# Optimization experiments

Measured on AMD Instinct MI355X. Metric: run time of the kernel, lower is better.

Reference implementation:

```python
import jax, jax.numpy as jnp
import numpy as np

N, E, NB, P = 100000, 1600000, 1000, 500000


def gcn_conv(x, edge_index, W, b):
    # PyG GCNConv: add self-loops, symmetric D^-1/2 (A+I) D^-1/2 normalization,
    # linear transform, bias.
    n = x.shape[0]
    loop = jnp.arange(n, dtype=edge_index.dtype)
    src = jnp.concatenate([edge_index[0], loop])
    dst = jnp.concatenate([edge_index[1], loop])
    deg = jax.ops.segment_sum(jnp.ones(src.shape[0], x.dtype), dst, num_segments=n)
    dinv = jnp.where(deg > 0, jax.lax.rsqrt(deg), 0.0)
    norm = dinv[src] * dinv[dst]                       # [E+n]
    xw = x @ W                                          # [n, out]
    out = jax.ops.segment_sum(xw[src] * norm[:, None], dst, num_segments=n)
    return out + b


def setup_inputs() -> dict:
    key = jax.random.key(0)
    ks = jax.random.split(key, 12)
    x = jax.random.normal(ks[0], (N, 27), jnp.float32)
    edge_index = jax.random.randint(ks[1], (2, E), 0, N, dtype=jnp.int32)
    bank = jax.random.normal(ks[2], (NB, 27), jnp.float32)
    node1 = jax.random.randint(ks[3], (P,), 0, N + NB, dtype=jnp.int32)
    node2 = jax.random.randint(ks[4], (P,), 0, N + NB, dtype=jnp.int32)

    def lin(k, fan_in, fan_out):
        s = 1.0 / np.sqrt(fan_in)
        kw, kb = jax.random.split(k)
        W = jax.random.uniform(kw, (fan_in, fan_out), jnp.float32, -s, s)
        b = jax.random.uniform(kb, (fan_out,), jnp.float32, -s, s)
        return W, b

    W1, b1 = lin(ks[5], 27, 60)
    W2, b2 = lin(ks[6], 60, 50)
    Wb, bb = lin(ks[7], 27, 50)
    Wf1, bf1 = lin(ks[8], 100, 40)
    Wf2, bf2 = lin(ks[9], 40, 20)
    Wf3, bf3 = lin(ks[10], 20, 4)
    return dict(x=x, bank=bank, W1=W1, b1=b1, W2=W2, b2=b2, Wb=Wb, bb=bb,
                Wf1=Wf1, bf1=bf1, Wf2=Wf2, bf2=bf2, Wf3=Wf3, bf3=bf3,
                edge_index=edge_index, node1=node1, node2=node2)


def reference(x, bank, W1, b1, W2, b2, Wb, bb, Wf1, bf1, Wf2, bf2, Wf3, bf3,
              edge_index, node1, node2):
    h = gcn_conv(x, edge_index, W1, b1)                 # [N, 60]
    h = gcn_conv(h, edge_index, W2, b2)                 # [N, 50]
    bk = bank @ Wb + bb                                 # [NB, 50]
    allh = jnp.concatenate([h, bk], axis=0)             # [N+NB, 50]
    z = jnp.concatenate([allh[node1], allh[node2]], axis=1)  # [P, 100]
    z = z @ Wf1 + bf1
    z = z @ Wf2 + bf2
    z = z @ Wf3 + bf3                                   # [P, 4]
    return jax.nn.softmax(z, axis=0)                    # softmax over dim 0, as in source
```

## Files before the change

### kernel.cpp

```cpp
#include <hip/hip_runtime.h>
#include <math.h>

#define N_NODES 100000
#define N_EDGES 1600000
#define NB_BANK 1000
#define N_PAIRS 500000

#define BUCK_SHIFT 8
#define BUCK_NODES 256
#define NBUCK 391
#define BCAP 5504
#define EPB 4096
#define NSCAT 391
#define NZB4 489
#define SMASK 0x1FFFF

struct Consts {
  float C[27*8];
  float Rb[27*8];
  float u[8];
  float vg[8];
  float vb[8];
};

__device__ void precompute_body(
    const float* __restrict__ W1, const float* __restrict__ b1,
    const float* __restrict__ W2, const float* __restrict__ b2,
    const float* __restrict__ Wb, const float* __restrict__ bb,
    const float* __restrict__ Wf1, const float* __restrict__ bf1,
    const float* __restrict__ Wf2, const float* __restrict__ bf2,
    const float* __restrict__ Wf3, const float* __restrict__ bf3,
    Consts* __restrict__ cst) {
  __shared__ float A[40*4];
  __shared__ float T[100*4];
  __shared__ float B[60*8];
  __shared__ float cvec[4];
  const int tid = threadIdx.x;
  const int nt = blockDim.x;

  for (int idx = tid; idx < 160; idx += nt) {
    int r = idx >> 2, k = idx & 3;
    float s = 0.f;
    for (int j = 0; j < 20; ++j) s += Wf2[r*20+j] * Wf3[j*4+k];
    A[idx] = s;
  }
  __syncthreads();
  for (int idx = tid; idx < 400; idx += nt) {
    int r = idx >> 2, k = idx & 3;
    float s = 0.f;
    for (int j = 0; j < 40; ++j) s += Wf1[r*40+j] * A[j*4+k];
    T[idx] = s;
  }
  if (tid < 4) {
    float s = bf3[tid];
    for (int j = 0; j < 40; ++j) s += bf1[j] * A[j*4+tid];
    for (int j = 0; j < 20; ++j) s += bf2[j] * Wf3[j*4+tid];
    cvec[tid] = s;
  }
  __syncthreads();
  for (int idx = tid; idx < 480; idx += nt) {
    int r = idx >> 3, k = idx & 7;
    int half = k >> 2, kk = k & 3;
    float s = 0.f;
    for (int j = 0; j < 50; ++j) s += W2[r*50+j] * T[(half*50+j)*4+kk];
    B[idx] = s;
  }
  __syncthreads();
  for (int idx = tid; idx < 456; idx += nt) {
    if (idx < 216) {
      int r = idx >> 3, k = idx & 7;
      float s = 0.f;
      for (int j = 0; j < 60; ++j) s += W1[r*60+j] * B[j*8+k];
      cst->C[idx] = s;
    } else if (idx < 432) {
      int i2 = idx - 216;
      int r = i2 >> 3, k = i2 & 7, half = k >> 2, kk = k & 3;
      float s = 0.f;
      for (int j = 0; j < 50; ++j) s += Wb[r*50+j] * T[(half*50+j)*4+kk];
      cst->Rb[i2] = s;
    } else if (idx < 440) {
      int k = idx - 432;
      float s = 0.f;
      for (int j = 0; j < 60; ++j) s += b1[j] * B[j*8+k];
      cst->u[k] = s;
    } else if (idx < 448) {
      int k = idx - 440, half = k >> 2, kk = k & 3;
      float s = (half == 0) ? cvec[kk] : 0.f;
      for (int j = 0; j < 50; ++j) s += b2[j] * T[(half*50+j)*4+kk];
      cst->vg[k] = s;
    } else {
      int k = idx - 448, half = k >> 2, kk = k & 3;
      float s = (half == 0) ? cvec[kk] : 0.f;
      for (int j = 0; j < 50; ++j) s += bb[j] * T[(half*50+j)*4+kk];
      cst->vb[k] = s;
    }
  }
}

__global__ __launch_bounds__(1024) void k_scatter(
    const int* __restrict__ ei, int* __restrict__ bcnt, int* __restrict__ ebuf,
    const float* __restrict__ W1, const float* __restrict__ b1,
    const float* __restrict__ W2, const float* __restrict__ b2,
    const float* __restrict__ Wb, const float* __restrict__ bb,
    const float* __restrict__ Wf1, const float* __restrict__ bf1,
    const float* __restrict__ Wf2, const float* __restrict__ bf2,
    const float* __restrict__ Wf3, const float* __restrict__ bf3,
    Consts* __restrict__ cst) {
  if (blockIdx.x == NSCAT) {
    precompute_body(W1, b1, W2, b2, Wb, bb, Wf1, bf1, Wf2, bf2, Wf3, bf3, cst);
    return;
  }
  __shared__ int hist[NBUCK];
  __shared__ int base[NBUCK];
  const int t = threadIdx.x;
  const int e0 = blockIdx.x * EPB;
  int dcache[EPB / 1024];
  if (t < NBUCK) hist[t] = 0;
  __syncthreads();
#pragma unroll
  for (int i = 0; i < EPB / 1024; ++i) {
    int e = e0 + i * 1024 + t;
    int d = (e < N_EDGES) ? ei[N_EDGES + e] : -1;
    dcache[i] = d;
    if (d >= 0) atomicAdd(&hist[d >> BUCK_SHIFT], 1);
  }
  __syncthreads();
  if (t < NBUCK) {
    int h = hist[t];
    base[t] = h ? (t * BCAP + atomicAdd(&bcnt[t], h)) : 0;
    hist[t] = 0;
  }
  __syncthreads();
#pragma unroll
  for (int i = 0; i < EPB / 1024; ++i) {
    int e = e0 + i * 1024 + t;
    int d = dcache[i];
    if (d >= 0) {
      int s = ei[e];
      int b = d >> BUCK_SHIFT;
      int pos = base[b] + atomicAdd(&hist[b], 1);
      ebuf[pos] = ((d & (BUCK_NODES - 1)) << 17) | s;
    }
  }
}

__global__ __launch_bounds__(512) void k_degfill_x8(
    const int* __restrict__ bcnt, const int* __restrict__ ebuf,
    const float* __restrict__ x, const Consts* __restrict__ cst,
    float* __restrict__ dinv, int* __restrict__ rbeg, int* __restrict__ rend,
    int* __restrict__ csr, float* __restrict__ Xs) {
  __shared__ int cnt[BUCK_NODES];
  __shared__ int lcur[BUCK_NODES];
  __shared__ float sdinv[BUCK_NODES];
  __shared__ float xs[BUCK_NODES * 27];
  const int b = blockIdx.x;
  const int t = threadIdx.x;
  if (t < BUCK_NODES) cnt[t] = 0;
  __syncthreads();
  const int beg = b * BCAP, end = beg + bcnt[b];
  for (int j = beg + t; j < end; j += 512)
    atomicAdd(&cnt[ebuf[j] >> 17], 1);
  const int xbase = b * (BUCK_NODES * 27);
  for (int j = t; j < BUCK_NODES * 27; j += 512) {
    int g = xbase + j;
    xs[j] = (g < N_NODES * 27) ? x[g] : 0.f;
  }
  __syncthreads();
  int v = (t < BUCK_NODES) ? cnt[t] : 0;
  for (int off = 1; off < BUCK_NODES; off <<= 1) {
    int u = (t < BUCK_NODES && t >= off) ? cnt[t - off] : 0;
    __syncthreads();
    if (t < BUCK_NODES) cnt[t] += u;
    __syncthreads();
  }
  if (t < BUCK_NODES) {
    const int node = (b << BUCK_SHIFT) + t;
    const int excl = beg + cnt[t] - v;
    lcur[t] = excl;
    float dv = rsqrtf((float)v + 1.0f);
    sdinv[t] = dv;
    if (node < N_NODES) {
      rbeg[node] = excl;
      rend[node] = excl + v;
      dinv[node] = dv;
    }
  }
  __syncthreads();
  for (int j = beg + t; j < end; j += 512) {
    int code = ebuf[j];
    int pos = atomicAdd(&lcur[code >> 17], 1);
    csr[pos] = code & SMASK;
  }
  for (int idx = t; idx < BUCK_NODES * 8; idx += 512) {
    int li = idx >> 3, k = idx & 7;
    int node = (b << BUCK_SHIFT) + li;
    if (node < N_NODES) {
      float s = 0.f;
      for (int c = 0; c < 27; ++c) s += xs[li*27+c] * cst->C[c*8+k];
      Xs[(size_t)node*8+k] = s * sdinv[li];
    }
  }
}

__global__ __launch_bounds__(256) void k_gather1(const int* __restrict__ rbeg,
                                                 const int* __restrict__ rend,
                                                 const int* __restrict__ csr,
                                                 const float* __restrict__ dinv,
                                                 const float2* __restrict__ Xs2,
                                                 float2* __restrict__ Ys2,
                                                 float* __restrict__ dvec) {
  int t = blockIdx.x * 256 + threadIdx.x;
  int d = t >> 2, q = t & 3;
  if (d >= N_NODES) return;
  const int beg = rbeg[d], end = rend[d];
  const float nd = dinv[d];
  float2 self = Xs2[d*4 + q];
  float ax = self.x, ay = self.y;
  float dsum = nd;
  int j = beg;
  for (; j + 8 <= end; j += 8) {
    int s0 = csr[j],   s1 = csr[j+1], s2 = csr[j+2], s3 = csr[j+3];
    int s4 = csr[j+4], s5 = csr[j+5], s6 = csr[j+6], s7 = csr[j+7];
    float2 a0 = Xs2[s0*4+q], a1 = Xs2[s1*4+q], a2 = Xs2[s2*4+q], a3 = Xs2[s3*4+q];
    float2 a4 = Xs2[s4*4+q], a5 = Xs2[s5*4+q], a6 = Xs2[s6*4+q], a7 = Xs2[s7*4+q];
    ax += ((a0.x + a1.x) + (a2.x + a3.x)) + ((a4.x + a5.x) + (a6.x + a7.x));
    ay += ((a0.y + a1.y) + (a2.y + a3.y)) + ((a4.y + a5.y) + (a6.y + a7.y));
    if (q == 0)
      dsum += ((dinv[s0] + dinv[s1]) + (dinv[s2] + dinv[s3]))
            + ((dinv[s4] + dinv[s5]) + (dinv[s6] + dinv[s7]));
  }
  for (; j < end; ++j) {
    int s = csr[j];
    float2 a = Xs2[s*4+q];
    ax += a.x; ay += a.y;
    if (q == 0) dsum += dinv[s];
  }
  float nn = nd * nd;
  Ys2[t] = make_float2(nn * ax, nn * ay);
  if (q == 0) dvec[d] = nd * dsum;
}

__global__ __launch_bounds__(256) void k_gather2g(const int* __restrict__ rbeg,
                                                  const int* __restrict__ rend,
                                                  const int* __restrict__ csr,
                                                  const float* __restrict__ dinv,
                                                  const float2* __restrict__ Ys2,
                                                  const float* __restrict__ dvec,
                                                  const float* __restrict__ bank,
                                                  const Consts* __restrict__ cst,
                                                  float2* __restrict__ gall2) {
  int t = blockIdx.x * 256 + threadIdx.x;
  int d = t >> 2, q = t & 3;
  if (d >= N_NODES + NB_BANK) return;
  int c0 = 2*q, c1 = 2*q + 1;
  if (d >= N_NODES) {
    int bk = d - N_NODES;
    float sx = cst->vb[c0], sy = cst->vb[c1];
    for (int cc = 0; cc < 27; ++cc) {
      float bv = bank[bk*27+cc];
      sx += bv * cst->Rb[cc*8+c0];
      sy += bv * cst->Rb[cc*8+c1];
    }
    gall2[t] = make_float2(sx, sy);
    return;
  }
  const int beg = rbeg[d], end = rend[d];
  float2 self = Ys2[d*4 + q];
  float ax = self.x, ay = self.y;
  int j = beg;
  for (; j + 8 <= end; j += 8) {
    int s0 = csr[j],   s1 = csr[j+1], s2 = csr[j+2], s3 = csr[j+3];
    int s4 = csr[j+4], s5 = csr[j+5], s6 = csr[j+6], s7 = csr[j+7];
    float2 a0 = Ys2[s0*4+q], a1 = Ys2[s1*4+q], a2 = Ys2[s2*4+q], a3 = Ys2[s3*4+q];
    float2 a4 = Ys2[s4*4+q], a5 = Ys2[s5*4+q], a6 = Ys2[s6*4+q], a7 = Ys2[s7*4+q];
    ax += ((a0.x + a1.x) + (a2.x + a3.x)) + ((a4.x + a5.x) + (a6.x + a7.x));
    ay += ((a0.y + a1.y) + (a2.y + a3.y)) + ((a4.y + a5.y) + (a6.y + a7.y));
  }
  for (; j < end; ++j) {
    float2 a = Ys2[csr[j]*4+q];
    ax += a.x; ay += a.y;
  }
  float nd = dinv[d], dv = dvec[d];
  gall2[t] = make_float2(nd * ax + dv * cst->u[c0] + cst->vg[c0],
                         nd * ay + dv * cst->u[c1] + cst->vg[c1]);
}

__device__ inline void sm_merge(float4& m1, float4& s1,
                                const float4 m2, const float4 s2) {
  float4 M;
  M.x = fmaxf(m1.x, m2.x); M.y = fmaxf(m1.y, m2.y);
  M.z = fmaxf(m1.z, m2.z); M.w = fmaxf(m1.w, m2.w);
  s1.x = s1.x * expf(m1.x - M.x) + s2.x * expf(m2.x - M.x);
  s1.y = s1.y * expf(m1.y - M.y) + s2.y * expf(m2.y - M.y);
  s1.z = s1.z * expf(m1.z - M.z) + s2.z * expf(m2.z - M.z);
  s1.w = s1.w * expf(m1.w - M.w) + s2.w * expf(m2.w - M.w);
  m1 = M;
}

__global__ __launch_bounds__(256) void k_z(const int* __restrict__ node1,
                                           const int* __restrict__ node2,
                                           const float* __restrict__ gall,
                                           float* __restrict__ z,
                                           float4* __restrict__ bs_m,
                                           float4* __restrict__ bs_s) {
  const int S = NZB4 * 256;
  int p0 = blockIdx.x * 256 + threadIdx.x;
  float4 m = make_float4(-1e30f, -1e30f, -1e30f, -1e30f);
  float4 s = make_float4(0.f, 0.f, 0.f, 0.f);
#pragma unroll
  for (int i = 0; i < 4; ++i) {
    int p = p0 + i * S;
    if (p < N_PAIRS) {
      int n1 = node1[p], n2 = node2[p];
      const float4 a = *(const float4*)(gall + (size_t)n1*8);
      const float4 b = *(const float4*)(gall + (size_t)n2*8 + 4);
      float4 zv = make_float4(a.x+b.x, a.y+b.y, a.z+b.z, a.w+b.w);
      ((float4*)z)[p] = zv;
      sm_merge(m, s, zv, make_float4(1.f, 1.f, 1.f, 1.f));
    }
  }
  __shared__ float4 lm[256], ls[256];
  lm[threadIdx.x] = m; ls[threadIdx.x] = s;
  __syncthreads();
  for (int st = 128; st > 0; st >>= 1) {
    if (threadIdx.x < st) {
      float4 mm = lm[threadIdx.x], ss = ls[threadIdx.x];
      sm_merge(mm, ss, lm[threadIdx.x + st], ls[threadIdx.x + st]);
      lm[threadIdx.x] = mm; ls[threadIdx.x] = ss;
    }
    __syncthreads();
  }
  if (threadIdx.x == 0) { bs_m[blockIdx.x] = lm[0]; bs_s[blockIdx.x] = ls[0]; }
}

__global__ __launch_bounds__(256) void k_final(const float* __restrict__ z,
                                               const float4* __restrict__ bs_m,
                                               const float4* __restrict__ bs_s,
                                               float* __restrict__ out) {
  float4 m = make_float4(-1e30f, -1e30f, -1e30f, -1e30f);
  float4 s = make_float4(0.f, 0.f, 0.f, 0.f);
  for (int i = threadIdx.x; i < NZB4; i += 256)
    sm_merge(m, s, bs_m[i], bs_s[i]);
  __shared__ float4 lm[256], ls[256];
  lm[threadIdx.x] = m; ls[threadIdx.x] = s;
  __syncthreads();
  for (int st = 128; st > 0; st >>= 1) {
    if (threadIdx.x < st) {
      float4 mm = lm[threadIdx.x], ss = ls[threadIdx.x];
      sm_merge(mm, ss, lm[threadIdx.x + st], ls[threadIdx.x + st]);
      lm[threadIdx.x] = mm; ls[threadIdx.x] = ss;
    }
    __syncthreads();
  }
  const float4 M = lm[0], S4 = ls[0];
  const float i0 = 1.f / S4.x, i1 = 1.f / S4.y;
  const float i2 = 1.f / S4.z, i3 = 1.f / S4.w;
  const int S = NZB4 * 256;
  int p0 = blockIdx.x * 256 + threadIdx.x;
#pragma unroll
  for (int i = 0; i < 4; ++i) {
    int p = p0 + i * S;
    if (p < N_PAIRS) {
      float4 zv = ((const float4*)z)[p];
      float4 o = make_float4(expf(zv.x - M.x) * i0, expf(zv.y - M.y) * i1,
                             expf(zv.z - M.z) * i2, expf(zv.w - M.w) * i3);
      ((float4*)out)[p] = o;
    }
  }
}

extern "C" void kernel_launch(void* const* d_in, const int* in_sizes, int n_in,
                              void* d_out, int out_size, void* d_ws, size_t ws_size,
                              hipStream_t stream) {
  const float* x    = (const float*)d_in[0];
  const float* bank = (const float*)d_in[1];
  const float* W1   = (const float*)d_in[2];
  const float* b1   = (const float*)d_in[3];
  const float* W2   = (const float*)d_in[4];
  const float* b2   = (const float*)d_in[5];
  const float* Wb   = (const float*)d_in[6];
  const float* bb   = (const float*)d_in[7];
  const float* Wf1  = (const float*)d_in[8];
  const float* bf1  = (const float*)d_in[9];
  const float* Wf2  = (const float*)d_in[10];
  const float* bf2  = (const float*)d_in[11];
  const float* Wf3  = (const float*)d_in[12];
  const float* bf3  = (const float*)d_in[13];
  const int* ei     = (const int*)d_in[14];
  const int* node1  = (const int*)d_in[15];
  const int* node2  = (const int*)d_in[16];
  float* out = (float*)d_out;

  char* w = (char*)d_ws;
  size_t off = 0;
  auto take = [&](size_t bytes) -> char* {
    char* p = w + off;
    off = (off + bytes + 255) & ~(size_t)255;
    return p;
  };
  Consts* cst    = (Consts*)take(sizeof(Consts));
  int*    bcnt   = (int*)take(NBUCK * 4);
  float*  dinv   = (float*)take(N_NODES * 4);
  int*    rbeg   = (int*)take(N_NODES * 4);
  int*    rend   = (int*)take(N_NODES * 4);
  int*    csr    = (int*)take((size_t)NBUCK * BCAP * 4);
  float*  Xs     = (float*)take((size_t)N_NODES * 8 * 4);
  float*  Ys     = (float*)take((size_t)N_NODES * 8 * 4);
  float*  dvec   = (float*)take(N_NODES * 4);
  float*  gall   = (float*)take((size_t)(N_NODES + NB_BANK) * 8 * 4);
  char*   shreg  = take((size_t)NBUCK * BCAP * 4 > (size_t)N_PAIRS * 16
                        ? (size_t)NBUCK * BCAP * 4 : (size_t)N_PAIRS * 16);
  int*    ebuf   = (int*)shreg;
  float*  z      = (float*)shreg;
  float4* bs_m   = (float4*)take((size_t)NZB4 * 16);
  float4* bs_s   = (float4*)take((size_t)NZB4 * 16);

  hipMemsetAsync(bcnt, 0, NBUCK * 4, stream);

  k_scatter<<<NSCAT + 1, 1024, 0, stream>>>(ei, bcnt, ebuf, W1, b1, W2, b2,
                                            Wb, bb, Wf1, bf1, Wf2, bf2,
                                            Wf3, bf3, cst);
  k_degfill_x8<<<NBUCK, 512, 0, stream>>>(bcnt, ebuf, x, cst,
                                          dinv, rbeg, rend, csr, Xs);
  k_gather1<<<(N_NODES * 4 + 255) / 256, 256, 0, stream>>>(
      rbeg, rend, csr, dinv, (const float2*)Xs, (float2*)Ys, dvec);
  k_gather2g<<<((N_NODES + NB_BANK) * 4 + 255) / 256, 256, 0, stream>>>(
      rbeg, rend, csr, dinv, (const float2*)Ys, dvec, bank, cst, (float2*)gall);
  k_z<<<NZB4, 256, 0, stream>>>(node1, node2, gall, z, bs_m, bs_s);
  k_final<<<NZB4, 256, 0, stream>>>(z, bs_m, bs_s, out);
}
```

Measured before the change: 202.6 us.

## Prefetch CSR indices in gathers and recompute z instead of storing it

The gather loops in both GCN aggregation kernels now load the next batch of eight CSR neighbour indices while the current batch's feature loads are in flight, so the index latency overlaps the feature gathers, and a 4-wide remainder step is added. The z buffer (500k float4) is no longer written by k_z and reread by k_final. k_final instead re-gathers node1/node2 rows from gall and recomputes z, trading an 8 MB write plus read for extra index and random gathers, which are likely cache-resident. It adds register pressure in the gather kernels.

```diff
diff --git a/kernel.cpp b/kernel.cpp
--- a/kernel.cpp
+++ b/kernel.cpp
@@ -218,16 +218,44 @@
   float ax = self.x, ay = self.y;
   float dsum = nd;
   int j = beg;
-  for (; j + 8 <= end; j += 8) {
+  if (j + 8 <= end) {
     int s0 = csr[j],   s1 = csr[j+1], s2 = csr[j+2], s3 = csr[j+3];
     int s4 = csr[j+4], s5 = csr[j+5], s6 = csr[j+6], s7 = csr[j+7];
-    float2 a0 = Xs2[s0*4+q], a1 = Xs2[s1*4+q], a2 = Xs2[s2*4+q], a3 = Xs2[s3*4+q];
-    float2 a4 = Xs2[s4*4+q], a5 = Xs2[s5*4+q], a6 = Xs2[s6*4+q], a7 = Xs2[s7*4+q];
-    ax += ((a0.x + a1.x) + (a2.x + a3.x)) + ((a4.x + a5.x) + (a6.x + a7.x));
-    ay += ((a0.y + a1.y) + (a2.y + a3.y)) + ((a4.y + a5.y) + (a6.y + a7.y));
-    if (q == 0)
-      dsum += ((dinv[s0] + dinv[s1]) + (dinv[s2] + dinv[s3]))
-            + ((dinv[s4] + dinv[s5]) + (dinv[s6] + dinv[s7]));
+    for (;;) {
+      float2 a0 = Xs2[s0*4+q], a1 = Xs2[s1*4+q], a2 = Xs2[s2*4+q], a3 = Xs2[s3*4+q];
+      float2 a4 = Xs2[s4*4+q], a5 = Xs2[s5*4+q], a6 = Xs2[s6*4+q], a7 = Xs2[s7*4+q];
+      float d0 = 0.f, d1 = 0.f, d2 = 0.f, d3 = 0.f;
+      float d4 = 0.f, d5 = 0.f, d6 = 0.f, d7 = 0.f;
+      if (q == 0) {
+        d0 = dinv[s0]; d1 = dinv[s1]; d2 = dinv[s2]; d3 = dinv[s3];
+        d4 = dinv[s4]; d5 = dinv[s5]; d6 = dinv[s6]; d7 = dinv[s7];
+      }
+      int jn = j + 8;
+      bool more = (jn + 8 <= end);
+      int u0, u1, u2, u3, u4, u5, u6, u7;
+      if (more) {
+        u0 = csr[jn];   u1 = csr[jn+1]; u2 = csr[jn+2]; u3 = csr[jn+3];
+        u4 = csr[jn+4]; u5 = csr[jn+5]; u6 = csr[jn+6]; u7 = csr[jn+7];
+      } else {
+        u0 = u1 = u2 = u3 = u4 = u5 = u6 = u7 = 0;
+      }
+      ax += ((a0.x + a1.x) + (a2.x + a3.x)) + ((a4.x + a5.x) + (a6.x + a7.x));
+      ay += ((a0.y + a1.y) + (a2.y + a3.y)) + ((a4.y + a5.y) + (a6.y + a7.y));
+      if (q == 0)
+        dsum += ((d0 + d1) + (d2 + d3)) + ((d4 + d5) + (d6 + d7));
+      j = jn;
+      if (!more) break;
+      s0 = u0; s1 = u1; s2 = u2; s3 = u3;
+      s4 = u4; s5 = u5; s6 = u6; s7 = u7;
+    }
+  }
+  if (j + 4 <= end) {
+    int a = csr[j], b = csr[j+1], c = csr[j+2], e = csr[j+3];
+    float2 p0 = Xs2[a*4+q], p1 = Xs2[b*4+q], p2 = Xs2[c*4+q], p3 = Xs2[e*4+q];
+    ax += (p0.x + p1.x) + (p2.x + p3.x);
+    ay += (p0.y + p1.y) + (p2.y + p3.y);
+    if (q == 0) dsum += (dinv[a] + dinv[b]) + (dinv[c] + dinv[e]);
+    j += 4;
   }
   for (; j < end; ++j) {
     int s = csr[j];
@@ -268,13 +296,35 @@
   float2 self = Ys2[d*4 + q];
   float ax = self.x, ay = self.y;
   int j = beg;
-  for (; j + 8 <= end; j += 8) {
+  if (j + 8 <= end) {
     int s0 = csr[j],   s1 = csr[j+1], s2 = csr[j+2], s3 = csr[j+3];
     int s4 = csr[j+4], s5 = csr[j+5], s6 = csr[j+6], s7 = csr[j+7];
-    float2 a0 = Ys2[s0*4+q], a1 = Ys2[s1*4+q], a2 = Ys2[s2*4+q], a3 = Ys2[s3*4+q];
-    float2 a4 = Ys2[s4*4+q], a5 = Ys2[s5*4+q], a6 = Ys2[s6*4+q], a7 = Ys2[s7*4+q];
-    ax += ((a0.x + a1.x) + (a2.x + a3.x)) + ((a4.x + a5.x) + (a6.x + a7.x));
-    ay += ((a0.y + a1.y) + (a2.y + a3.y)) + ((a4.y + a5.y) + (a6.y + a7.y));
+    for (;;) {
+      float2 a0 = Ys2[s0*4+q], a1 = Ys2[s1*4+q], a2 = Ys2[s2*4+q], a3 = Ys2[s3*4+q];
+      float2 a4 = Ys2[s4*4+q], a5 = Ys2[s5*4+q], a6 = Ys2[s6*4+q], a7 = Ys2[s7*4+q];
+      int jn = j + 8;
+      bool more = (jn + 8 <= end);
+      int u0, u1, u2, u3, u4, u5, u6, u7;
+      if (more) {
+        u0 = csr[jn];   u1 = csr[jn+1]; u2 = csr[jn+2]; u3 = csr[jn+3];
+        u4 = csr[jn+4]; u5 = csr[jn+5]; u6 = csr[jn+6]; u7 = csr[jn+7];
+      } else {
+        u0 = u1 = u2 = u3 = u4 = u5 = u6 = u7 = 0;
+      }
+      ax += ((a0.x + a1.x) + (a2.x + a3.x)) + ((a4.x + a5.x) + (a6.x + a7.x));
+      ay += ((a0.y + a1.y) + (a2.y + a3.y)) + ((a4.y + a5.y) + (a6.y + a7.y));
+      j = jn;
+      if (!more) break;
+      s0 = u0; s1 = u1; s2 = u2; s3 = u3;
+      s4 = u4; s5 = u5; s6 = u6; s7 = u7;
+    }
+  }
+  if (j + 4 <= end) {
+    int a = csr[j], b = csr[j+1], c = csr[j+2], e = csr[j+3];
+    float2 p0 = Ys2[a*4+q], p1 = Ys2[b*4+q], p2 = Ys2[c*4+q], p3 = Ys2[e*4+q];
+    ax += (p0.x + p1.x) + (p2.x + p3.x);
+    ay += (p0.y + p1.y) + (p2.y + p3.y);
+    j += 4;
   }
   for (; j < end; ++j) {
     float2 a = Ys2[csr[j]*4+q];
@@ -300,7 +350,6 @@
 __global__ __launch_bounds__(256) void k_z(const int* __restrict__ node1,
                                            const int* __restrict__ node2,
                                            const float* __restrict__ gall,
-                                           float* __restrict__ z,
                                            float4* __restrict__ bs_m,
                                            float4* __restrict__ bs_s) {
   const int S = NZB4 * 256;
@@ -315,7 +364,6 @@
       const float4 a = *(const float4*)(gall + (size_t)n1*8);
       const float4 b = *(const float4*)(gall + (size_t)n2*8 + 4);
       float4 zv = make_float4(a.x+b.x, a.y+b.y, a.z+b.z, a.w+b.w);
-      ((float4*)z)[p] = zv;
       sm_merge(m, s, zv, make_float4(1.f, 1.f, 1.f, 1.f));
     }
   }
@@ -333,7 +381,9 @@
   if (threadIdx.x == 0) { bs_m[blockIdx.x] = lm[0]; bs_s[blockIdx.x] = ls[0]; }
 }
 
-__global__ __launch_bounds__(256) void k_final(const float* __restrict__ z,
+__global__ __launch_bounds__(256) void k_final(const int* __restrict__ node1,
+                                               const int* __restrict__ node2,
+                                               const float* __restrict__ gall,
                                                const float4* __restrict__ bs_m,
                                                const float4* __restrict__ bs_s,
                                                float* __restrict__ out) {
@@ -361,7 +411,10 @@
   for (int i = 0; i < 4; ++i) {
     int p = p0 + i * S;
     if (p < N_PAIRS) {
-      float4 zv = ((const float4*)z)[p];
+      int n1 = node1[p], n2 = node2[p];
+      const float4 a = *(const float4*)(gall + (size_t)n1*8);
+      const float4 b = *(const float4*)(gall + (size_t)n2*8 + 4);
+      float4 zv = make_float4(a.x+b.x, a.y+b.y, a.z+b.z, a.w+b.w);
       float4 o = make_float4(expf(zv.x - M.x) * i0, expf(zv.y - M.y) * i1,
                              expf(zv.z - M.z) * i2, expf(zv.w - M.w) * i3);
       ((float4*)out)[p] = o;
@@ -408,10 +461,7 @@
   float*  Ys     = (float*)take((size_t)N_NODES * 8 * 4);
   float*  dvec   = (float*)take(N_NODES * 4);
   float*  gall   = (float*)take((size_t)(N_NODES + NB_BANK) * 8 * 4);
-  char*   shreg  = take((size_t)NBUCK * BCAP * 4 > (size_t)N_PAIRS * 16
-                        ? (size_t)NBUCK * BCAP * 4 : (size_t)N_PAIRS * 16);
-  int*    ebuf   = (int*)shreg;
-  float*  z      = (float*)shreg;
+  int*    ebuf   = (int*)take((size_t)NBUCK * BCAP * 4);
   float4* bs_m   = (float4*)take((size_t)NZB4 * 16);
   float4* bs_s   = (float4*)take((size_t)NZB4 * 16);
 
@@ -426,6 +476,6 @@
       rbeg, rend, csr, dinv, (const float2*)Xs, (float2*)Ys, dvec);
   k_gather2g<<<((N_NODES + NB_BANK) * 4 + 255) / 256, 256, 0, stream>>>(
       rbeg, rend, csr, dinv, (const float2*)Ys, dvec, bank, cst, (float2*)gall);
-  k_z<<<NZB4, 256, 0, stream>>>(node1, node2, gall, z, bs_m, bs_s);
-  k_final<<<NZB4, 256, 0, stream>>>(z, bs_m, bs_s, out);
-}
+  k_z<<<NZB4, 256, 0, stream>>>(node1, node2, gall, bs_m, bs_s);
+  k_final<<<NZB4, 256, 0, stream>>>(node1, node2, gall, bs_m, bs_s, out);
+}
```

Result: no change. 202.2 us (-0.2%).
